# Performance work log

Hardware: AMD Instinct MI355X
Metric: run time of the kernel (lower is better)

Reference implementation:

```python
import jax, jax.numpy as jnp
import numpy as np

COMMITMENT_WEIGHT = 1.0


def setup_inputs() -> dict:
    key = jax.random.key(0)
    k1, k2 = jax.random.split(key)
    clap_embeddings = jax.random.normal(k1, (16, 2048, 512), dtype=jnp.float32)
    # Learned codebooks for the 8 residual quantizer stages: [Q, C, D]
    codebooks = jax.random.normal(k2, (8, 1024, 512), dtype=jnp.float32)
    return {"clap_embeddings": clap_embeddings, "codebooks": codebooks}


def reference(clap_embeddings, codebooks):
    """Residual VQ: cascade of nearest-codebook lookups on the residual.
    Returns (quantized [B,T,D], indices [B,T,Q], commit_loss scalar)."""
    B, T, D = clap_embeddings.shape
    flat = clap_embeddings.reshape(-1, D)  # [N, D], N = B*T

    def step(carry, cb):
        residual, quant_acc = carry          # [N,D], [N,D]; cb: [C,D]
        cb_sq = jnp.sum(cb * cb, axis=-1)    # [C]
        # squared-dist argmin: ||r||^2 term is constant per row, drop it
        dists = cb_sq[None, :] - 2.0 * (residual @ cb.T)  # [N, C]
        idx = jnp.argmin(dists, axis=-1)     # [N]
        qv = cb[idx]                         # [N, D] gather
        # commitment loss: mse(detach(quantize), residual_input)
        loss = jnp.mean(jnp.square(jax.lax.stop_gradient(qv) - residual))
        # straight-through estimator
        qv_st = residual + jax.lax.stop_gradient(qv - residual)
        new_residual = residual - jax.lax.stop_gradient(qv)
        return (new_residual, quant_acc + qv_st), (idx, loss)

    init = (flat, jnp.zeros_like(flat))
    (_, quant_flat), (idx_q, losses) = jax.lax.scan(step, init, codebooks)

    quantized = quant_flat.reshape(B, T, D)
    indices = jnp.transpose(idx_q, (1, 0)).reshape(B, T, -1)  # [B, T, Q]
    commit_loss = jnp.sum(losses) * COMMITMENT_WEIGHT
    return quantized, indices, commit_loss
```

## Files before the change

### kernel.cpp

```cpp
#include <hip/hip_runtime.h>
#include <hip/hip_bf16.h>

#define NQ 8
#define NC 1024
#define ND 512
#define NROWTOT 32768
#define QOFF 16777216ULL

typedef short short8 __attribute__((ext_vector_type(8)));
typedef float f32x16 __attribute__((ext_vector_type(16)));

__device__ __forceinline__ unsigned f2bf_u(float f) {
  unsigned u = __float_as_uint(f);
  return (u + 0x7FFFu + ((u >> 16) & 1u)) >> 16;
}
__device__ __forceinline__ unsigned pack_hl(float x) {
  unsigned hb = f2bf_u(x);
  float hf = __uint_as_float(hb << 16);
  unsigned lb = f2bf_u(x - hf);
  return (hb << 16) | lb;
}
__device__ __forceinline__ void merge_in(float &d1, int &i1, float &d2, int &i2,
                                         float nd, int ni) {
  bool b1 = (nd < d1) || (nd == d1 && ni < i1);
  bool b2 = (nd < d2) || (nd == d2 && ni < i2);
  if (b1) { d2 = d1; i2 = i1; d1 = nd; i1 = ni; }
  else if (b2) { d2 = nd; i2 = ni; }
}

__global__ __launch_bounds__(256) void cbsq_kernel(const float* __restrict__ cbg,
                                                   float* __restrict__ ws) {
  const int tid = threadIdx.x, wv = tid >> 6, lane = tid & 63;
  const int cbase = blockIdx.x * 32 + wv * 8;
  for (int j = 0; j < 8; ++j) {
    const int c = cbase + j;
    const float4* p = reinterpret_cast<const float4*>(cbg + (size_t)c * ND + lane * 8);
    float4 a = p[0], b = p[1];
    float s = a.x*a.x + a.y*a.y + a.z*a.z + a.w*a.w
            + b.x*b.x + b.y*b.y + b.z*b.z + b.w*b.w;
    #pragma unroll
    for (int m = 1; m < 64; m <<= 1) s += __shfl_xor(s, m, 64);
    if (lane == 0) ws[c] = s;
  }
}

__global__ __launch_bounds__(256) void fmt_kernel(const float* __restrict__ cbg,
                                                  unsigned short* __restrict__ Bh,
                                                  unsigned short* __restrict__ Bl) {
  int t = blockIdx.x * 256 + threadIdx.x;
  int i16 = t & 1023, ks = (t >> 10) & 31, cp = (t >> 15) & 1, q = (t >> 16) & 7;
  int grp = i16 >> 9, col = i16 & 511, c = cp * 512 + col;
  const float* src = cbg + ((size_t)q * NC + c) * ND + ks * 16 + grp * 8;
  float4 a = reinterpret_cast<const float4*>(src)[0];
  float4 b = reinterpret_cast<const float4*>(src)[1];
  float v[8] = {a.x, a.y, a.z, a.w, b.x, b.y, b.z, b.w};
  unsigned short hv[8], lv[8];
  #pragma unroll
  for (int j = 0; j < 8; ++j) {
    unsigned hb = f2bf_u(v[j]);
    float hf = __uint_as_float(hb << 16);
    unsigned lb = f2bf_u(v[j] - hf);
    hv[j] = (unsigned short)hb; lv[j] = (unsigned short)lb;
  }
  int phys = i16 ^ ((i16 >> 3) & 7);
  size_t dst = (size_t)(t >> 10) * 8192 + (size_t)phys * 8;
  uint4 wh, wl;
  wh.x = hv[0] | ((unsigned)hv[1] << 16); wh.y = hv[2] | ((unsigned)hv[3] << 16);
  wh.z = hv[4] | ((unsigned)hv[5] << 16); wh.w = hv[6] | ((unsigned)hv[7] << 16);
  wl.x = lv[0] | ((unsigned)lv[1] << 16); wl.y = lv[2] | ((unsigned)lv[3] << 16);
  wl.z = lv[4] | ((unsigned)lv[5] << 16); wl.w = lv[6] | ((unsigned)lv[7] << 16);
  *reinterpret_cast<uint4*>(Bh + dst) = wh;
  *reinterpret_cast<uint4*>(Bl + dst) = wl;
}

#define ROWS64 64
#define TAU2 0.02f

__global__ __launch_bounds__(256, 1) void rvq_mfma(
    const float* __restrict__ emb, const float* __restrict__ cbg,
    const float* __restrict__ cbsq_g, float* __restrict__ lossws,
    const unsigned short* __restrict__ Bh, const unsigned short* __restrict__ Bl,
    float* __restrict__ outf) {
  __shared__ unsigned resU[ND * ROWS64];
  __shared__ float mrgd[2][2][ROWS64][2];
  __shared__ int   mrgi[2][2][ROWS64][2];
  __shared__ int   idx_all[NQ][ROWS64];
  __shared__ int   fi_sh[ROWS64];
  __shared__ int   tlist[ROWS64][3];
  __shared__ int   tcount;
  __shared__ float wred[4];

  const int tid = threadIdx.x;
  const int w = tid >> 6, l = tid & 63;
  const int n0 = blockIdx.x * ROWS64;
  const int rowbase = (w >> 1) * 32;
  const int colq = (w & 1) * 256;
  const int arow = rowbase + (l & 31);
  const int phase = blockIdx.x & 31;
  const int cpswap = (blockIdx.x >> 5) & 1;

  union U8 { uint4 q4; short8 s; unsigned u[4]; };

  {
    const int row = tid & 63, kp = (tid >> 6) * 128;
    const float4* src = reinterpret_cast<const float4*>(emb + (size_t)(n0 + row) * ND + kp);
    #pragma unroll 4
    for (int i = 0; i < 32; ++i) {
      float4 v = src[i];
      int k = kp + i * 4;
      resU[(k + 0) * ROWS64 + row] = pack_hl(v.x);
      resU[(k + 1) * ROWS64 + row] = pack_hl(v.y);
      resU[(k + 2) * ROWS64 + row] = pack_hl(v.z);
      resU[(k + 3) * ROWS64 + row] = pack_hl(v.w);
    }
  }

  int baddr[8];
  #pragma unroll
  for (int t = 0; t < 8; ++t) {
    int i16 = ((l >> 5) << 9) + colq + t * 32 + (l & 31);
    baddr[t] = (i16 ^ ((i16 >> 3) & 7)) * 8;
  }
  __syncthreads();

  for (int q = 0; q < NQ; ++q) {
    if (tid == 0) tcount = 0;

    #pragma unroll 1
    for (int cpi = 0; cpi < 2; ++cpi) {
      const int cp = cpi ^ cpswap;
      f32x16 acc[8];
      #pragma unroll
      for (int t = 0; t < 8; ++t)
        #pragma unroll
        for (int e = 0; e < 16; ++e) acc[t][e] = 0.f;

      const unsigned short* bhc = Bh + (size_t)((q * 2 + cp) * 32) * 8192;
      const unsigned short* blc = Bl + (size_t)((q * 2 + cp) * 32) * 8192;
      uint4 fA[16], fB[16];
      unsigned uaA[8], uaB[8];

      float sqv[8];
      #pragma unroll
      for (int t = 0; t < 8; ++t)
        sqv[t] = cbsq_g[q * NC + cp * 512 + colq + t * 32 + (l & 31)];

#define KS(i) (((i) + phase) & 31)

#define LOADB(buf, kk) { \
      const unsigned short* _h = bhc + (size_t)(kk) * 8192; \
      const unsigned short* _l = blc + (size_t)(kk) * 8192; \
      _Pragma("unroll") \
      for (int t = 0; t < 8; ++t) { \
        buf[t]     = *reinterpret_cast<const uint4*>(_h + baddr[t]); \
        buf[8 + t] = *reinterpret_cast<const uint4*>(_l + baddr[t]); \
      } }

#define READA(ua, kk) { \
      const int _k0 = (kk) * 16 + ((l >> 5) << 3); \
      _Pragma("unroll") \
      for (int j = 0; j < 8; ++j) ua[j] = resU[(_k0 + j) * ROWS64 + arow]; }

#define MFMAS(ua, buf) { \
      U8 ah, al; \
      _Pragma("unroll") \
      for (int p2 = 0; p2 < 4; ++p2) { \
        ah.u[p2] = (ua[2*p2] >> 16) | (ua[2*p2+1] & 0xFFFF0000u); \
        al.u[p2] = (ua[2*p2] & 0xFFFFu) | (ua[2*p2+1] << 16); \
      } \
      _Pragma("unroll") \
      for (int t = 0; t < 8; ++t) { \
        U8 bh_, bl_; bh_.q4 = buf[t]; bl_.q4 = buf[8 + t]; \
        acc[t] = __builtin_amdgcn_mfma_f32_32x32x16_bf16(ah.s, bh_.s, acc[t], 0, 0, 0); \
        acc[t] = __builtin_amdgcn_mfma_f32_32x32x16_bf16(al.s, bh_.s, acc[t], 0, 0, 0); \
        acc[t] = __builtin_amdgcn_mfma_f32_32x32x16_bf16(ah.s, bl_.s, acc[t], 0, 0, 0); \
      } }

      {
        const int k00 = KS(0);
        LOADB(fA, k00); READA(uaA, k00);
      }
      #pragma unroll 1
      for (int ks = 0; ks < 32; ks += 2) {
        const int k1 = KS(ks + 1);
        LOADB(fB, k1); READA(uaB, k1);
        MFMAS(uaA, fA);
        const int kn = KS(ks + 2 < 32 ? ks + 2 : 0);
        LOADB(fA, kn); READA(uaA, kn);
        MFMAS(uaB, fB);
      }
#undef LOADB
#undef READA
#undef MFMAS
#undef KS

      #pragma unroll
      for (int rg2 = 0; rg2 < 16; ++rg2) {
        float d1 = INFINITY, d2 = INFINITY; int i1 = 0x7fffffff, i2 = 0x7fffffff;
        #pragma unroll
        for (int t = 0; t < 8; ++t) {
          int col = cp * 512 + colq + t * 32 + (l & 31);
          float dd = sqv[t] - 2.0f * acc[t][rg2];
          merge_in(d1, i1, d2, i2, dd, col);
        }
        #pragma unroll
        for (int m = 1; m < 32; m <<= 1) {
          float od1 = __shfl_xor(d1, m, 64), od2 = __shfl_xor(d2, m, 64);
          int oi1 = __shfl_xor(i1, m, 64), oi2 = __shfl_xor(i2, m, 64);
          merge_in(d1, i1, d2, i2, od1, oi1);
          merge_in(d1, i1, d2, i2, od2, oi2);
        }
        if ((l & 31) == 0) {
          int h = l >> 5;
          int row = rowbase + (rg2 & 3) + 8 * (rg2 >> 2) + 4 * h;
          mrgd[cp][w & 1][row][0] = d1; mrgd[cp][w & 1][row][1] = d2;
          mrgi[cp][w & 1][row][0] = i1; mrgi[cp][w & 1][row][1] = i2;
        }
      }
    }
    __syncthreads();

    if (tid < ROWS64) {
      float d1 = INFINITY, d2 = INFINITY; int i1 = 0x7fffffff, i2 = 0x7fffffff;
      #pragma unroll
      for (int c2 = 0; c2 < 2; ++c2)
        #pragma unroll
        for (int s2 = 0; s2 < 2; ++s2) {
          merge_in(d1, i1, d2, i2, mrgd[c2][s2][tid][0], mrgi[c2][s2][tid][0]);
          merge_in(d1, i1, d2, i2, mrgd[c2][s2][tid][1], mrgi[c2][s2][tid][1]);
        }
      int fi = i1 < 0 ? 0 : (i1 > NC - 1 ? NC - 1 : i1);
      int ib = i2 < 0 ? 0 : (i2 > NC - 1 ? NC - 1 : i2);
      fi_sh[tid] = fi;
      if (d2 - d1 < TAU2 && ib != fi) {
        int p = atomicAdd(&tcount, 1);
        tlist[p][0] = tid; tlist[p][1] = fi; tlist[p][2] = ib;
      }
    }
    __syncthreads();

    {
      int nt_ = tcount;
      for (int it = w; it < nt_; it += 4) {
        int row = tlist[it][0], ia = tlist[it][1], ib = tlist[it][2];
        float rr[8];
        const float4* ep = reinterpret_cast<const float4*>(emb + (size_t)(n0 + row) * ND + l * 8);
        float4 e0 = ep[0], e1 = ep[1];
        rr[0]=e0.x; rr[1]=e0.y; rr[2]=e0.z; rr[3]=e0.w;
        rr[4]=e1.x; rr[5]=e1.y; rr[6]=e1.z; rr[7]=e1.w;
        for (int t2 = 0; t2 < q; ++t2) {
          const float4* cr = reinterpret_cast<const float4*>(
              cbg + ((size_t)t2 * NC + idx_all[t2][row]) * ND + l * 8);
          float4 c0 = cr[0], c1 = cr[1];
          rr[0]-=c0.x; rr[1]-=c0.y; rr[2]-=c0.z; rr[3]-=c0.w;
          rr[4]-=c1.x; rr[5]-=c1.y; rr[6]-=c1.z; rr[7]-=c1.w;
        }
        double da = 0.0, db = 0.0;
        {
          const float4* cr = reinterpret_cast<const float4*>(
              cbg + ((size_t)q * NC + ia) * ND + l * 8);
          float4 c0 = cr[0], c1 = cr[1];
          float cv[8] = {c0.x,c0.y,c0.z,c0.w,c1.x,c1.y,c1.z,c1.w};
          #pragma unroll
          for (int j = 0; j < 8; ++j) { double e = (double)cv[j] - (double)rr[j]; da += e * e; }
        }
        {
          const float4* cr = reinterpret_cast<const float4*>(
              cbg + ((size_t)q * NC + ib) * ND + l * 8);
          float4 c0 = cr[0], c1 = cr[1];
          float cv[8] = {c0.x,c0.y,c0.z,c0.w,c1.x,c1.y,c1.z,c1.w};
          #pragma unroll
          for (int j = 0; j < 8; ++j) { double e = (double)cv[j] - (double)rr[j]; db += e * e; }
        }
        #pragma unroll
        for (int m = 1; m < 64; m <<= 1) { da += __shfl_xor(da, m, 64); db += __shfl_xor(db, m, 64); }
        if (l == 0 && (db < da || (db == da && ib < ia))) fi_sh[row] = ib;
      }
    }
    __syncthreads();

    if (tid < ROWS64) {
      idx_all[q][tid] = fi_sh[tid];
      outf[QOFF + (size_t)(n0 + tid) * NQ + q] = (float)fi_sh[tid];
    }

    {
      const int row = tid & 63, kp = (tid >> 6) * 128;
      const float* crow = cbg + ((size_t)q * NC + fi_sh[row]) * ND;
      const float4* cp4 = reinterpret_cast<const float4*>(crow + kp);
      const float4* ep4 = reinterpret_cast<const float4*>(emb + (size_t)(n0 + row) * ND + kp);
      float4* op4 = reinterpret_cast<float4*>(outf + (size_t)(n0 + row) * ND + kp);
      float ls = 0.f;
      #pragma unroll 1
      for (int i0 = 0; i0 < 32; i0 += 8) {
        float4 cv8[8], ev8[8];
        #pragma unroll
        for (int u2 = 0; u2 < 8; ++u2) cv8[u2] = cp4[i0 + u2];
        if (q == NQ - 1) {
          #pragma unroll
          for (int u2 = 0; u2 < 8; ++u2) ev8[u2] = ep4[i0 + u2];
        }
        #pragma unroll
        for (int u2 = 0; u2 < 8; ++u2) {
          const int i = i0 + u2;
          const int k = kp + i * 4;
          float x[4]; float cc4[4] = {cv8[u2].x, cv8[u2].y, cv8[u2].z, cv8[u2].w};
          #pragma unroll
          for (int j = 0; j < 4; ++j) {
            unsigned u = resU[(k + j) * ROWS64 + row];
            float r = __uint_as_float(u & 0xFFFF0000u) + __uint_as_float(u << 16);
            x[j] = r - cc4[j];
            resU[(k + j) * ROWS64 + row] = pack_hl(x[j]);
            ls += x[j] * x[j];
          }
          if (q == NQ - 1) {
            float4 qv;
            qv.x = ev8[u2].x - x[0]; qv.y = ev8[u2].y - x[1];
            qv.z = ev8[u2].z - x[2]; qv.w = ev8[u2].w - x[3];
            op4[i] = qv;
          }
        }
      }
      #pragma unroll
      for (int m = 1; m < 64; m <<= 1) ls += __shfl_xor(ls, m, 64);
      if (l == 0) wred[w] = ls;
    }
    __syncthreads();
    if (tid == 0) lossws[blockIdx.x * NQ + q] = wred[0] + wred[1] + wred[2] + wred[3];
    __syncthreads();
  }
}

#define ROWS 32
#define BK 32
#define CP 512
#define TAU 0.05f

__global__ __launch_bounds__(256, 1) void rvq_fb(
    const float* __restrict__ emb, const float* __restrict__ cbg,
    const float* __restrict__ cbsq, float* __restrict__ lossws,
    float* __restrict__ outf) {
  __shared__ float resT[ND][ROWS];
  __shared__ float cc[BK][CP];
  __shared__ int   idx_sh[ROWS];
  __shared__ float wred[4];

  const int tid = threadIdx.x;
  const int wv = tid >> 6, lane = tid & 63;
  const int rg = wv, cg = lane;
  const int n0 = blockIdx.x * ROWS;

  float qacc[64];
  #pragma unroll
  for (int s = 0; s < 64; ++s) qacc[s] = 0.f;

  {
    const int r = tid & 31, db = tid >> 5;
    const float4* src = reinterpret_cast<const float4*>(emb + (size_t)(n0 + r) * ND + db * 64);
    #pragma unroll
    for (int s = 0; s < 16; ++s) {
      float4 v = src[s];
      int d = db * 64 + s * 4;
      resT[d+0][r] = v.x; resT[d+1][r] = v.y; resT[d+2][r] = v.z; resT[d+3][r] = v.w;
    }
  }
  __syncthreads();

  const int c0l = cg * 8;
  const int swm = (c0l >> 6) << 2;
  const int off0 = c0l ^ swm;
  const int off1 = (c0l + 4) ^ swm;

  for (int q = 0; q < NQ; ++q) {
    const float* cbq = cbg + (size_t)q * NC * ND;
    float bd1[8], bd2[8]; int bi1[8], bi2[8];
    #pragma unroll
    for (int j = 0; j < 8; ++j) { bd1[j]=INFINITY; bd2[j]=INFINITY; bi1[j]=0x7fffffff; bi2[j]=0x7fffffff; }

    for (int cp = 0; cp < 2; ++cp) {
      float acc[8][8];
      #pragma unroll
      for (int a = 0; a < 8; ++a)
        #pragma unroll
        for (int b = 0; b < 8; ++b) acc[a][b] = 0.f;

      for (int kc = 0; kc < ND / BK; ++kc) {
        __syncthreads();
        {
          const int half = tid & 1;
          const int k0 = half * 16;
          #pragma unroll
          for (int it = 0; it < 4; ++it) {
            const int c = (tid >> 1) + it * 128;
            const int pc = c ^ ((c >> 6) << 2);
            const float4* src = reinterpret_cast<const float4*>(
                cbq + (size_t)(cp * CP + c) * ND + kc * BK + half * 16);
            float4 v0 = src[0], v1 = src[1], v2 = src[2], v3 = src[3];
            cc[k0+ 0][pc]=v0.x; cc[k0+ 1][pc]=v0.y; cc[k0+ 2][pc]=v0.z; cc[k0+ 3][pc]=v0.w;
            cc[k0+ 4][pc]=v1.x; cc[k0+ 5][pc]=v1.y; cc[k0+ 6][pc]=v1.z; cc[k0+ 7][pc]=v1.w;
            cc[k0+ 8][pc]=v2.x; cc[k0+ 9][pc]=v2.y; cc[k0+10][pc]=v2.z; cc[k0+11][pc]=v2.w;
            cc[k0+12][pc]=v3.x; cc[k0+13][pc]=v3.y; cc[k0+14][pc]=v3.z; cc[k0+15][pc]=v3.w;
          }
        }
        __syncthreads();

        float tmp[8][8];
        #pragma unroll
        for (int a = 0; a < 8; ++a)
          #pragma unroll
          for (int b = 0; b < 8; ++b) tmp[a][b] = 0.f;

        #pragma unroll
        for (int kk = 0; kk < BK; ++kk) {
          const float4* rp = reinterpret_cast<const float4*>(&resT[kc * BK + kk][rg * 8]);
          float4 r0 = rp[0], r1 = rp[1];
          const float* ccrow = &cc[kk][0];
          float4 c0 = *reinterpret_cast<const float4*>(ccrow + off0);
          float4 c1 = *reinterpret_cast<const float4*>(ccrow + off1);
          float rv[8] = {r0.x, r0.y, r0.z, r0.w, r1.x, r1.y, r1.z, r1.w};
          float cv[8] = {c0.x, c0.y, c0.z, c0.w, c1.x, c1.y, c1.z, c1.w};
          #pragma unroll
          for (int a = 0; a < 8; ++a)
            #pragma unroll
            for (int b = 0; b < 8; ++b)
              tmp[a][b] = fmaf(rv[a], cv[b], tmp[a][b]);
        }
        #pragma unroll
        for (int a = 0; a < 8; ++a)
          #pragma unroll
          for (int b = 0; b < 8; ++b) acc[a][b] += tmp[a][b];
      }

      const float4* qp = reinterpret_cast<const float4*>(cbsq + q * NC + cp * CP + cg * 8);
      float4 s0 = qp[0], s1 = qp[1];
      float sqv[8] = {s0.x, s0.y, s0.z, s0.w, s1.x, s1.y, s1.z, s1.w};
      #pragma unroll
      for (int r = 0; r < 8; ++r) {
        float d1 = INFINITY, d2 = INFINITY; int i1 = 0x7fffffff, i2 = 0x7fffffff;
        #pragma unroll
        for (int j = 0; j < 8; ++j) {
          float dd = sqv[j] - 2.0f * acc[r][j];
          merge_in(d1, i1, d2, i2, dd, cp * CP + cg * 8 + j);
        }
        #pragma unroll
        for (int m = 1; m < 64; m <<= 1) {
          float od1 = __shfl_xor(d1, m, 64), od2 = __shfl_xor(d2, m, 64);
          int oi1 = __shfl_xor(i1, m, 64), oi2 = __shfl_xor(i2, m, 64);
          merge_in(d1, i1, d2, i2, od1, oi1);
          merge_in(d1, i1, d2, i2, od2, oi2);
        }
        merge_in(bd1[r], bi1[r], bd2[r], bi2[r], d1, i1);
        merge_in(bd1[r], bi1[r], bd2[r], bi2[r], d2, i2);
      }
    }

    #pragma unroll 1
    for (int r = 0; r < 8; ++r) {
      int fi = bi1[r];
      if (bd2[r] - bd1[r] < TAU) {
        const int row = rg * 8 + r;
        const int ia = bi1[r], ib = bi2[r];
        double da = 0.0, db2 = 0.0;
        #pragma unroll 1
        for (int t = 0; t < 2; ++t) {
          const int cidx = t ? ib : ia;
          const float* cr = cbq + (size_t)cidx * ND;
          double dot = 0.0, ss = 0.0;
          #pragma unroll
          for (int u = 0; u < 8; ++u) {
            int k = lane * 8 + u;
            double cvv = (double)cr[k];
            double rvv = (double)resT[k][row];
            dot += cvv * rvv; ss += cvv * cvv;
          }
          #pragma unroll
          for (int m = 1; m < 64; m <<= 1) { dot += __shfl_xor(dot, m, 64); ss += __shfl_xor(ss, m, 64); }
          double dd = ss - 2.0 * dot;
          if (t) db2 = dd; else da = dd;
        }
        if (db2 < da || (db2 == da && ib < ia)) fi = ib;
      }
      fi = fi < 0 ? 0 : (fi > NC - 1 ? NC - 1 : fi);
      if (lane == 0) {
        idx_sh[rg * 8 + r] = fi;
        outf[QOFF + (size_t)(n0 + rg * 8 + r) * NQ + q] = (float)fi;
      }
    }
    __syncthreads();

    {
      const int r = tid & 31, db = tid >> 5;
      const float* crow = cbq + (size_t)idx_sh[r] * ND;
      float ls = 0.f;
      #pragma unroll
      for (int s = 0; s < 64; ++s) {
        int d = db * 64 + s;
        float cv = crow[d];
        float nv = resT[d][r] - cv;
        resT[d][r] = nv;
        qacc[s] += cv;
        ls += nv * nv;
      }
      #pragma unroll
      for (int m = 1; m < 64; m <<= 1) ls += __shfl_xor(ls, m, 64);
      if (lane == 0) wred[wv] = ls;
    }
    __syncthreads();
    if (tid == 0) lossws[blockIdx.x * NQ + q] = wred[0] + wred[1] + wred[2] + wred[3];
    __syncthreads();
  }

  {
    const int r = tid & 31, db = tid >> 5;
    #pragma unroll
    for (int g = 0; g < 16; ++g) {
      float4 w2;
      w2.x = qacc[g*4+0]; w2.y = qacc[g*4+1]; w2.z = qacc[g*4+2]; w2.w = qacc[g*4+3];
      *reinterpret_cast<float4*>(outf + (size_t)(n0 + r) * ND + db * 64 + g * 4) = w2;
    }
  }
}

__global__ __launch_bounds__(256) void loss_kernel(const float* __restrict__ lossws,
                                                   int n, float* __restrict__ outf) {
  __shared__ float red[256];
  const int tid = threadIdx.x;
  float s = 0.f;
  for (int i = tid; i < n; i += 256) s += lossws[i];
  red[tid] = s;
  __syncthreads();
  for (int w = 128; w > 0; w >>= 1) {
    if (tid < w) red[tid] += red[tid + w];
    __syncthreads();
  }
  if (tid == 0) outf[QOFF + (size_t)NROWTOT * NQ] = red[0] / 16777216.0f;
}

extern "C" void kernel_launch(void* const* d_in, const int* in_sizes, int n_in,
                              void* d_out, int out_size, void* d_ws, size_t ws_size,
                              hipStream_t stream) {
  (void)in_sizes; (void)n_in; (void)out_size;
  const float* emb = (const float*)d_in[0];
  const float* cbg = (const float*)d_in[1];
  float* wsf = (float*)d_ws;
  float* outf = (float*)d_out;

  cbsq_kernel<<<256, 256, 0, stream>>>(cbg, wsf);

  if (ws_size >= (size_t)18 * 1024 * 1024) {
    unsigned short* Bh = (unsigned short*)((char*)d_ws + 65536);
    unsigned short* Bl = Bh + 4194304;
    fmt_kernel<<<2048, 256, 0, stream>>>(cbg, Bh, Bl);
    rvq_mfma<<<512, 256, 0, stream>>>(emb, cbg, wsf, wsf + 8192, Bh, Bl, outf);
    loss_kernel<<<1, 256, 0, stream>>>(wsf + 8192, 4096, outf);
  } else {
    rvq_fb<<<1024, 256, 0, stream>>>(emb, cbg, wsf, wsf + 8192, outf);
    loss_kernel<<<1, 256, 0, stream>>>(wsf + 8192, 8192, outf);
  }
}
```

Measured before the change: 4.085 ms.

## Widen rvq_mfma blocks to 16 waves, splitting codebook columns eight ways

The MFMA residual-VQ kernel now runs 1024 threads per block instead of 256. Each wave covers 64 codebook columns instead of 256, so it holds 2 accumulator tiles rather than 8. The cross-wave argmin merge grows to 8 column slices, and the residual load/update loops are re-partitioned over 16 waves. The aim is more waves per CU to hide latency and lower per-wave register pressure. The cost is more LDS merge traffic, redundant A-fragment reads from shared memory by each wave, and heavier block-wide barriers. The launch bound (1024,4) asks for 4 blocks per SM, which LDS size may not allow.

Result: faster. 3.943 ms (-3.5%).

```diff
diff --git a/kernel.cpp b/kernel.cpp
--- a/kernel.cpp
+++ b/kernel.cpp
@@ -76,25 +76,25 @@
 #define ROWS64 64
 #define TAU2 0.02f
 
-__global__ __launch_bounds__(256, 1) void rvq_mfma(
+__global__ __launch_bounds__(1024, 4) void rvq_mfma(
     const float* __restrict__ emb, const float* __restrict__ cbg,
     const float* __restrict__ cbsq_g, float* __restrict__ lossws,
     const unsigned short* __restrict__ Bh, const unsigned short* __restrict__ Bl,
     float* __restrict__ outf) {
   __shared__ unsigned resU[ND * ROWS64];
-  __shared__ float mrgd[2][2][ROWS64][2];
-  __shared__ int   mrgi[2][2][ROWS64][2];
+  __shared__ float mrgd[2][8][ROWS64][2];
+  __shared__ int   mrgi[2][8][ROWS64][2];
   __shared__ int   idx_all[NQ][ROWS64];
   __shared__ int   fi_sh[ROWS64];
   __shared__ int   tlist[ROWS64][3];
   __shared__ int   tcount;
-  __shared__ float wred[4];
+  __shared__ float wred[16];
 
   const int tid = threadIdx.x;
   const int w = tid >> 6, l = tid & 63;
   const int n0 = blockIdx.x * ROWS64;
-  const int rowbase = (w >> 1) * 32;
-  const int colq = (w & 1) * 256;
+  const int rowbase = (w >> 3) * 32;
+  const int colq = (w & 7) * 64;
   const int arow = rowbase + (l & 31);
   const int phase = blockIdx.x & 31;
   const int cpswap = (blockIdx.x >> 5) & 1;
@@ -102,22 +102,24 @@
   union U8 { uint4 q4; short8 s; unsigned u[4]; };
 
   {
-    const int row = tid & 63, kp = (tid >> 6) * 128;
+    const int row = tid & 63, kp = (tid >> 6) * 32;
     const float4* src = reinterpret_cast<const float4*>(emb + (size_t)(n0 + row) * ND + kp);
-    #pragma unroll 4
-    for (int i = 0; i < 32; ++i) {
-      float4 v = src[i];
+    float4 v8[8];
+    #pragma unroll
+    for (int i = 0; i < 8; ++i) v8[i] = src[i];
+    #pragma unroll
+    for (int i = 0; i < 8; ++i) {
       int k = kp + i * 4;
-      resU[(k + 0) * ROWS64 + row] = pack_hl(v.x);
-      resU[(k + 1) * ROWS64 + row] = pack_hl(v.y);
-      resU[(k + 2) * ROWS64 + row] = pack_hl(v.z);
-      resU[(k + 3) * ROWS64 + row] = pack_hl(v.w);
-    }
-  }
-
-  int baddr[8];
+      resU[(k + 0) * ROWS64 + row] = pack_hl(v8[i].x);
+      resU[(k + 1) * ROWS64 + row] = pack_hl(v8[i].y);
+      resU[(k + 2) * ROWS64 + row] = pack_hl(v8[i].z);
+      resU[(k + 3) * ROWS64 + row] = pack_hl(v8[i].w);
+    }
+  }
+
+  int baddr[2];
   #pragma unroll
-  for (int t = 0; t < 8; ++t) {
+  for (int t = 0; t < 2; ++t) {
     int i16 = ((l >> 5) << 9) + colq + t * 32 + (l & 31);
     baddr[t] = (i16 ^ ((i16 >> 3) & 7)) * 8;
   }
@@ -129,20 +131,20 @@
     #pragma unroll 1
     for (int cpi = 0; cpi < 2; ++cpi) {
       const int cp = cpi ^ cpswap;
-      f32x16 acc[8];
-      #pragma unroll
-      for (int t = 0; t < 8; ++t)
+      f32x16 acc[2];
+      #pragma unroll
+      for (int t = 0; t < 2; ++t)
         #pragma unroll
         for (int e = 0; e < 16; ++e) acc[t][e] = 0.f;
 
       const unsigned short* bhc = Bh + (size_t)((q * 2 + cp) * 32) * 8192;
       const unsigned short* blc = Bl + (size_t)((q * 2 + cp) * 32) * 8192;
-      uint4 fA[16], fB[16];
+      uint4 fA[4], fB[4];
       unsigned uaA[8], uaB[8];
 
-      float sqv[8];
-      #pragma unroll
-      for (int t = 0; t < 8; ++t)
+      float sqv[2];
+      #pragma unroll
+      for (int t = 0; t < 2; ++t)
         sqv[t] = cbsq_g[q * NC + cp * 512 + colq + t * 32 + (l & 31)];
 
 #define KS(i) (((i) + phase) & 31)
@@ -151,9 +153,9 @@
       const unsigned short* _h = bhc + (size_t)(kk) * 8192; \
       const unsigned short* _l = blc + (size_t)(kk) * 8192; \
       _Pragma("unroll") \
-      for (int t = 0; t < 8; ++t) { \
+      for (int t = 0; t < 2; ++t) { \
         buf[t]     = *reinterpret_cast<const uint4*>(_h + baddr[t]); \
-        buf[8 + t] = *reinterpret_cast<const uint4*>(_l + baddr[t]); \
+        buf[2 + t] = *reinterpret_cast<const uint4*>(_l + baddr[t]); \
       } }
 
 #define READA(ua, kk) { \
@@ -169,8 +171,8 @@
         al.u[p2] = (ua[2*p2] & 0xFFFFu) | (ua[2*p2+1] << 16); \
       } \
       _Pragma("unroll") \
-      for (int t = 0; t < 8; ++t) { \
-        U8 bh_, bl_; bh_.q4 = buf[t]; bl_.q4 = buf[8 + t]; \
+      for (int t = 0; t < 2; ++t) { \
+        U8 bh_, bl_; bh_.q4 = buf[t]; bl_.q4 = buf[2 + t]; \
         acc[t] = __builtin_amdgcn_mfma_f32_32x32x16_bf16(ah.s, bh_.s, acc[t], 0, 0, 0); \
         acc[t] = __builtin_amdgcn_mfma_f32_32x32x16_bf16(al.s, bh_.s, acc[t], 0, 0, 0); \
         acc[t] = __builtin_amdgcn_mfma_f32_32x32x16_bf16(ah.s, bl_.s, acc[t], 0, 0, 0); \
@@ -198,7 +200,7 @@
       for (int rg2 = 0; rg2 < 16; ++rg2) {
         float d1 = INFINITY, d2 = INFINITY; int i1 = 0x7fffffff, i2 = 0x7fffffff;
         #pragma unroll
-        for (int t = 0; t < 8; ++t) {
+        for (int t = 0; t < 2; ++t) {
           int col = cp * 512 + colq + t * 32 + (l & 31);
           float dd = sqv[t] - 2.0f * acc[t][rg2];
           merge_in(d1, i1, d2, i2, dd, col);
@@ -213,8 +215,8 @@
         if ((l & 31) == 0) {
           int h = l >> 5;
           int row = rowbase + (rg2 & 3) + 8 * (rg2 >> 2) + 4 * h;
-          mrgd[cp][w & 1][row][0] = d1; mrgd[cp][w & 1][row][1] = d2;
-          mrgi[cp][w & 1][row][0] = i1; mrgi[cp][w & 1][row][1] = i2;
+          mrgd[cp][w & 7][row][0] = d1; mrgd[cp][w & 7][row][1] = d2;
+          mrgi[cp][w & 7][row][0] = i1; mrgi[cp][w & 7][row][1] = i2;
         }
       }
     }
@@ -225,7 +227,7 @@
       #pragma unroll
       for (int c2 = 0; c2 < 2; ++c2)
         #pragma unroll
-        for (int s2 = 0; s2 < 2; ++s2) {
+        for (int s2 = 0; s2 < 8; ++s2) {
           merge_in(d1, i1, d2, i2, mrgd[c2][s2][tid][0], mrgi[c2][s2][tid][0]);
           merge_in(d1, i1, d2, i2, mrgd[c2][s2][tid][1], mrgi[c2][s2][tid][1]);
         }
@@ -241,7 +243,7 @@
 
     {
       int nt_ = tcount;
-      for (int it = w; it < nt_; it += 4) {
+      for (int it = w; it < nt_; it += 16) {
         int row = tlist[it][0], ia = tlist[it][1], ib = tlist[it][2];
         float rr[8];
         const float4* ep = reinterpret_cast<const float4*>(emb + (size_t)(n0 + row) * ND + l * 8);
@@ -285,40 +287,36 @@
     }
 
     {
-      const int row = tid & 63, kp = (tid >> 6) * 128;
+      const int row = tid & 63, kp = (tid >> 6) * 32;
       const float* crow = cbg + ((size_t)q * NC + fi_sh[row]) * ND;
       const float4* cp4 = reinterpret_cast<const float4*>(crow + kp);
       const float4* ep4 = reinterpret_cast<const float4*>(emb + (size_t)(n0 + row) * ND + kp);
       float4* op4 = reinterpret_cast<float4*>(outf + (size_t)(n0 + row) * ND + kp);
       float ls = 0.f;
-      #pragma unroll 1
-      for (int i0 = 0; i0 < 32; i0 += 8) {
-        float4 cv8[8], ev8[8];
-        #pragma unroll
-        for (int u2 = 0; u2 < 8; ++u2) cv8[u2] = cp4[i0 + u2];
+      float4 cv8[8], ev8[8];
+      #pragma unroll
+      for (int u2 = 0; u2 < 8; ++u2) cv8[u2] = cp4[u2];
+      if (q == NQ - 1) {
+        #pragma unroll
+        for (int u2 = 0; u2 < 8; ++u2) ev8[u2] = ep4[u2];
+      }
+      #pragma unroll
+      for (int u2 = 0; u2 < 8; ++u2) {
+        const int k = kp + u2 * 4;
+        float x[4]; float cc4[4] = {cv8[u2].x, cv8[u2].y, cv8[u2].z, cv8[u2].w};
+        #pragma unroll
+        for (int j = 0; j < 4; ++j) {
+          unsigned u = resU[(k + j) * ROWS64 + row];
+          float r = __uint_as_float(u & 0xFFFF0000u) + __uint_as_float(u << 16);
+          x[j] = r - cc4[j];
+          resU[(k + j) * ROWS64 + row] = pack_hl(x[j]);
+          ls += x[j] * x[j];
+        }
         if (q == NQ - 1) {
-          #pragma unroll
-          for (int u2 = 0; u2 < 8; ++u2) ev8[u2] = ep4[i0 + u2];
-        }
-        #pragma unroll
-        for (int u2 = 0; u2 < 8; ++u2) {
-          const int i = i0 + u2;
-          const int k = kp + i * 4;
-          float x[4]; float cc4[4] = {cv8[u2].x, cv8[u2].y, cv8[u2].z, cv8[u2].w};
-          #pragma unroll
-          for (int j = 0; j < 4; ++j) {
-            unsigned u = resU[(k + j) * ROWS64 + row];
-            float r = __uint_as_float(u & 0xFFFF0000u) + __uint_as_float(u << 16);
-            x[j] = r - cc4[j];
-            resU[(k + j) * ROWS64 + row] = pack_hl(x[j]);
-            ls += x[j] * x[j];
-          }
-          if (q == NQ - 1) {
-            float4 qv;
-            qv.x = ev8[u2].x - x[0]; qv.y = ev8[u2].y - x[1];
-            qv.z = ev8[u2].z - x[2]; qv.w = ev8[u2].w - x[3];
-            op4[i] = qv;
-          }
+          float4 qv;
+          qv.x = ev8[u2].x - x[0]; qv.y = ev8[u2].y - x[1];
+          qv.z = ev8[u2].z - x[2]; qv.w = ev8[u2].w - x[3];
+          op4[u2] = qv;
         }
       }
       #pragma unroll
@@ -326,7 +324,12 @@
       if (l == 0) wred[w] = ls;
     }
     __syncthreads();
-    if (tid == 0) lossws[blockIdx.x * NQ + q] = wred[0] + wred[1] + wred[2] + wred[3];
+    if (tid == 0) {
+      float s = 0.f;
+      #pragma unroll
+      for (int i = 0; i < 16; ++i) s += wred[i];
+      lossws[blockIdx.x * NQ + q] = s;
+    }
     __syncthreads();
   }
 }
@@ -551,7 +554,7 @@
     unsigned short* Bh = (unsigned short*)((char*)d_ws + 65536);
     unsigned short* Bl = Bh + 4194304;
     fmt_kernel<<<2048, 256, 0, stream>>>(cbg, Bh, Bl);
-    rvq_mfma<<<512, 256, 0, stream>>>(emb, cbg, wsf, wsf + 8192, Bh, Bl, outf);
+    rvq_mfma<<<512, 1024, 0, stream>>>(emb, cbg, wsf, wsf + 8192, Bh, Bl, outf);
     loss_kernel<<<1, 256, 0, stream>>>(wsf + 8192, 4096, outf);
   } else {
     rvq_fb<<<1024, 256, 0, stream>>>(emb, cbg, wsf, wsf + 8192, outf);
```
